# Kernel optimization log

Hardware: AMD Instinct MI355X
Metric: run time of the kernel (lower is better)

## Reference

```python
import jax, jax.numpy as jnp
import numpy as np
from jax import lax

IOU_THRESHOLD = 0.5       # init kwarg
MAX_BOX_PRE_NMS = 1000    # hardcoded in original forward


def _iou_one_vs_all(box, boxes):
    # box: [4] xyxy, boxes: [K,4] xyxy  (torchvision-style IoU, no +1)
    lt = jnp.maximum(box[:2], boxes[:, :2])
    rb = jnp.minimum(box[2:], boxes[:, 2:])
    wh = jnp.clip(rb - lt, 0.0)
    inter = wh[:, 0] * wh[:, 1]
    area1 = (box[2] - box[0]) * (box[3] - box[1])
    area2 = (boxes[:, 2] - boxes[:, 0]) * (boxes[:, 3] - boxes[:, 1])
    return inter / (area1 + area2 - inter)


def _nms_keep(boxes, valid, iou_thr):
    # boxes [K,4] sorted by descending score, valid [K] bool. Greedy NMS:
    # suppress any later box with IoU > iou_thr w.r.t. a kept box.
    K = boxes.shape[0]
    idx = jnp.arange(K)

    def body(i, keep):
        iou = _iou_one_vs_all(boxes[i], boxes)          # [K]
        alive = keep[i] & valid[i]
        suppress = alive & (iou > iou_thr) & (idx > i)
        return keep & ~suppress

    return lax.fori_loop(0, K, body, valid)


def setup_inputs() -> dict:
    key = jax.random.key(0)
    ks = jax.random.split(key, 6)
    B, A, C = 4, 100000, 80
    x = jax.random.normal(ks[0], (B, 3, 64, 64), jnp.float32)
    anchors = jax.random.uniform(ks[1], (1, A, 4), dtype=jnp.float32)
    regression = jax.random.normal(ks[2], (B, A, 4), jnp.float32)
    classification = jax.random.uniform(ks[3], (B, A, C), dtype=jnp.float32)
    # valid xyxy boxes: x2>x1, y2>y1
    xy = jax.random.uniform(ks[4], (B, A, 2), dtype=jnp.float32) * 512.0
    wh = jax.random.uniform(ks[5], (B, A, 2), dtype=jnp.float32) * 64.0 + 1.0
    transformed_anchors = jnp.concatenate([xy, xy + wh], axis=-1)
    return {
        "x": x,
        "anchors": anchors,
        "regression": regression,
        "classification": classification,
        "transformed_anchors": transformed_anchors,
        "threshold": jnp.float32(0.5),
        "max_box": 100,
    }


def reference(x, anchors, regression, classification, transformed_anchors, threshold, max_box):
    # Padded, jit-compatible equivalent of the per-image/per-class loop:
    # rois [B,max_box,4], scores [B,max_box] (0 for padding),
    # class_ids [B,max_box] (-1 for padding).
    B, A, C = classification.shape
    K = MAX_BOX_PRE_NMS
    # threshold gate -> -inf so below-threshold candidates never survive top-k
    scores = jnp.where(classification > threshold, classification, -jnp.inf)  # [B,A,C]
    scores_ct = jnp.swapaxes(scores, 1, 2)                                    # [B,C,A]
    top_s, top_idx = lax.top_k(scores_ct, K)                                  # [B,C,K]
    boxes = jnp.take_along_axis(
        transformed_anchors[:, None], top_idx[..., None], axis=2)             # [B,C,K,4]
    valid = jnp.isfinite(top_s)                                               # [B,C,K]

    keep = jax.vmap(lambda b, v: _nms_keep(b, v, IOU_THRESHOLD))(
        boxes.reshape(B * C, K, 4), valid.reshape(B * C, K)).reshape(B, C, K)

    kept_scores = jnp.where(keep, top_s, -jnp.inf)
    flat_scores = kept_scores.reshape(B, C * K)
    flat_boxes = boxes.reshape(B, C * K, 4)
    class_ids = jnp.broadcast_to(
        jnp.arange(C, dtype=jnp.int32)[:, None], (C, K)).reshape(C * K)

    fin_s, fin_i = lax.top_k(flat_scores, max_box)                            # [B,max_box]
    rois = jnp.take_along_axis(flat_boxes, fin_i[..., None], axis=1)          # [B,max_box,4]
    out_class = class_ids[fin_i]
    out_valid = jnp.isfinite(fin_s)
    rois = jnp.where(out_valid[..., None], rois, 0.0)
    scores_out = jnp.where(out_valid, fin_s, 0.0)
    out_class = jnp.where(out_valid, out_class, -1)
    return rois, scores_out, out_class
```

## Files before the change

### kernel.cpp

```cpp
#include <hip/hip_runtime.h>
#include <hip/hip_bf16.h>

typedef unsigned long long u64;

#define KNMS 1000
#define KP   1024
#define CAP  4096
#define NBIN 8192
#define SLICES 320
#define SCAP 32
#define SLOTS (SLICES*SCAP)
#define CMAX 128
#define FSEL 1024
#define IOU_THR 0.5f

#define NEGINF __uint_as_float(0xFF800000u)


__device__ __forceinline__ void find_cutoff(unsigned int* hist, int nbins,
    unsigned int* csum, int nthreads, int tid, unsigned int rank,
    unsigned int* s_bin, unsigned int* s_gt, unsigned int* s_total, int* s_all) {
  int chunk = nbins / nthreads;
  unsigned int cs = 0;
  int base = tid * chunk;
  for (int q = 0; q < chunk; q++) cs += hist[base + q];
  csum[tid] = cs;
  __syncthreads();
  if (tid == 0) {
    unsigned int total = 0;
    for (int ch = 0; ch < nthreads; ch++) total += csum[ch];
    *s_total = total;
    if (total <= rank) { *s_bin = 0u; *s_gt = 0u; *s_all = 1; }
    else {
      unsigned int acc = 0; int ch = nthreads - 1;
      while (acc + csum[ch] < rank) { acc += csum[ch]; ch--; }
      int bin = ch * chunk + chunk - 1;
      while (acc + hist[bin] < rank) { acc += hist[bin]; bin--; }
      *s_bin = (unsigned)bin; *s_gt = acc; *s_all = 0;
    }
  }
  __syncthreads();
}

template<int N, int NT>
__device__ __forceinline__ void bitonic_desc(u64* a, int tid) {
  for (int k = 2; k <= N; k <<= 1) {
    for (int j = k >> 1; j > 0; j >>= 1) {
      for (int t = tid; t < N; t += NT) {
        int ixj = t ^ j;
        if (ixj > t) {
          u64 x = a[t], y = a[ixj];
          if (((t & k) == 0) ? (x < y) : (x > y)) { a[t] = y; a[ixj] = x; }
        }
      }
      __syncthreads();
    }
  }
}

__device__ __forceinline__ bool iou_gt(float4 bi, float ai, float4 bj, float aj) {
  float ltx = fmaxf(bi.x, bj.x), lty = fmaxf(bi.y, bj.y);
  float rbx = fminf(bi.z, bj.z), rby = fminf(bi.w, bj.w);
  float ww = fmaxf(rbx - ltx, 0.f), hh = fmaxf(rby - lty, 0.f);
  float inter = ww * hh;
  float uni = (ai + aj) - inter;
  float q = (inter + inter) - uni;
  float t = uni * 0x1p-24f;
  return q > t;
}

__global__ __launch_bounds__(1024) void k_sample(const float* __restrict__ cls,
    const float* __restrict__ thr_p, unsigned* __restrict__ gcut,
    float* __restrict__ gatef, unsigned* __restrict__ gflag, int A, int C) {
  int b = blockIdx.x, tid = threadIdx.x;
  __shared__ unsigned hist[CMAX * 64];
  float thr = *thr_p;
  unsigned base_bin = __float_as_uint(thr) >> 18;
  for (int i = tid; i < C * 64; i += 1024) hist[i] = 0u;
  __syncthreads();
  const float* src = cls + (size_t)b * A * C;
  const int NS = 4096;
  if ((C & 3) == 0) {
    int C4 = C >> 2;
    const float4* s4 = (const float4*)src;
    int tot4 = NS * C4;
    for (int idx = tid; idx < tot4; idx += 1024) {
      int s = idx / C4, c4 = idx - s * C4;
      int a = (int)(((long long)s * A) >> 12);
      float4 v = s4[(size_t)a * C4 + c4];
      float vv[4] = {v.x, v.y, v.z, v.w};
#pragma unroll
      for (int q = 0; q < 4; q++) {
        float sv = vv[q];
        if (sv > thr) {
          unsigned rel = (__float_as_uint(sv) >> 18) - base_bin;
          if (rel > 63u) rel = 63u;
          atomicAdd(&hist[(c4 * 4 + q) * 64 + rel], 1u);
        }
      }
    }
  } else {
    int tot = NS * C;
    for (int idx = tid; idx < tot; idx += 1024) {
      int s = idx / C, c = idx - s * C;
      int a = (int)(((long long)s * A) >> 12);
      float sv = src[(size_t)a * C + c];
      if (sv > thr) {
        unsigned rel = (__float_as_uint(sv) >> 18) - base_bin;
        if (rel > 63u) rel = 63u;
        atomicAdd(&hist[c * 64 + rel], 1u);
      }
    }
  }
  __syncthreads();
  if (tid < C) {
    int ns = NS < A ? NS : A;
    long long r = (1500LL * ns) / A; if (r < 1) r = 1;
    unsigned acc = 0; int bin = -1;
    for (int rb = 63; rb >= 0; --rb) {
      acc += hist[tid * 64 + rb];
      if (acc >= (unsigned)r) { bin = rb; break; }
    }
    unsigned cutv = (bin < 0) ? 0u : (base_bin + (unsigned)bin);
    gcut[b * C + tid] = cutv;
    float gate = thr;
    if (cutv != 0u) {
      unsigned cb = cutv << 18;
      if (__uint_as_float(cb) > thr) gate = __uint_as_float(cb - 1u);
    }
    gatef[b * C + tid] = gate;
    gflag[b * C + tid] = 0u;
  }
}

__global__ void k_selA(const float* __restrict__ cls,
    const float* __restrict__ gatef, u64* __restrict__ gcand,
    unsigned* __restrict__ gpc, unsigned* __restrict__ gflag, int A, int C) {
  int slice = blockIdx.x, b = blockIdx.y, tid = threadIdx.x;
  int nt = blockDim.x;
  __shared__ u64 stage[CMAX * SCAP];
  __shared__ unsigned pcnt[CMAX];
  int C4 = C >> 2;
  for (int i = tid; i < C; i += nt) pcnt[i] = 0u;
  __syncthreads();
  int ANC = (A + SLICES - 1) / SLICES;
  int a0 = slice * ANC, a1 = min(A, a0 + ANC);
  int c4 = tid % C4;
  int r0 = tid / C4;
  int R = nt / C4;
  float4 g4 = ((const float4*)(gatef + (size_t)b * C))[c4];
  const float4* p = (const float4*)cls + (size_t)b * A * C4
                    + (size_t)(a0 + r0) * C4 + c4;
  int cb = c4 << 2;
  for (int ar = a0 + r0; ar < a1; ar += R, p += (size_t)R * C4) {
    float4 v = *p;
    bool p0 = v.x > g4.x, p1 = v.y > g4.y, p2 = v.z > g4.z, p3 = v.w > g4.w;
    if (p0 | p1 | p2 | p3) {
      unsigned ia = (unsigned)(~(unsigned)ar);
      if (p0) { unsigned pos = atomicAdd(&pcnt[cb + 0], 1u);
        if (pos < SCAP) stage[(cb + 0) * SCAP + pos] = ((u64)__float_as_uint(v.x) << 32) | ia; }
      if (p1) { unsigned pos = atomicAdd(&pcnt[cb + 1], 1u);
        if (pos < SCAP) stage[(cb + 1) * SCAP + pos] = ((u64)__float_as_uint(v.y) << 32) | ia; }
      if (p2) { unsigned pos = atomicAdd(&pcnt[cb + 2], 1u);
        if (pos < SCAP) stage[(cb + 2) * SCAP + pos] = ((u64)__float_as_uint(v.z) << 32) | ia; }
      if (p3) { unsigned pos = atomicAdd(&pcnt[cb + 3], 1u);
        if (pos < SCAP) stage[(cb + 3) * SCAP + pos] = ((u64)__float_as_uint(v.w) << 32) | ia; }
    }
  }
  __syncthreads();
  for (int idx = tid; idx < C * SCAP; idx += nt) {
    int c = idx >> 5, j = idx & (SCAP - 1);
    unsigned cnt2 = pcnt[c]; if (cnt2 > SCAP) cnt2 = SCAP;
    if ((unsigned)j < cnt2)
      gcand[(size_t)(b * C + c) * SLOTS + slice * SCAP + j] = stage[idx];
  }
  for (int c = tid; c < C; c += nt) {
    unsigned cnt2 = pcnt[c];
    if (cnt2 > SCAP) { atomicOr(&gflag[b * C + c], 1u); cnt2 = SCAP; }
    gpc[(size_t)(b * C + c) * SLICES + slice] = cnt2;
  }
}

__global__ void k_selAs(const float* __restrict__ cls,
    const float* __restrict__ gatef, u64* __restrict__ gcand,
    unsigned* __restrict__ gpc, unsigned* __restrict__ gflag, int A, int C) {
  int slice = blockIdx.x, b = blockIdx.y, tid = threadIdx.x;
  int nt = blockDim.x;
  __shared__ u64 stage[CMAX * SCAP];
  __shared__ unsigned pcnt[CMAX];
  for (int i = tid; i < C; i += nt) pcnt[i] = 0u;
  __syncthreads();
  int ANC = (A + SLICES - 1) / SLICES;
  int a0 = slice * ANC, a1 = min(A, a0 + ANC);
  int c = tid % C;
  int r0 = tid / C;
  int R = nt / C;
  float gate = gatef[(size_t)b * C + c];
  const float* p = cls + (size_t)b * A * C + (size_t)(a0 + r0) * C + c;
  for (int ar = a0 + r0; ar < a1; ar += R, p += (size_t)R * C) {
    float sv = *p;
    if (sv > gate) {
      unsigned pos = atomicAdd(&pcnt[c], 1u);
      if (pos < SCAP)
        stage[c * SCAP + pos] = ((u64)__float_as_uint(sv) << 32) | (unsigned)(~(unsigned)ar);
    }
  }
  __syncthreads();
  for (int idx = tid; idx < C * SCAP; idx += nt) {
    int cc = idx >> 5, j = idx & (SCAP - 1);
    unsigned cnt2 = pcnt[cc]; if (cnt2 > SCAP) cnt2 = SCAP;
    if ((unsigned)j < cnt2)
      gcand[(size_t)(b * C + cc) * SLOTS + slice * SCAP + j] = stage[idx];
  }
  for (int cc = tid; cc < C; cc += nt) {
    unsigned cnt2 = pcnt[cc];
    if (cnt2 > SCAP) { atomicOr(&gflag[b * C + cc], 1u); cnt2 = SCAP; }
    gpc[(size_t)(b * C + cc) * SLICES + slice] = cnt2;
  }
}

__global__ __launch_bounds__(1024) void k_selB(const u64* __restrict__ gcand,
    const unsigned* __restrict__ gpc, const unsigned* __restrict__ gcut,
    const unsigned* __restrict__ gflag, const float* __restrict__ cls,
    const float* __restrict__ thr_p, const float* __restrict__ tanch,
    float* __restrict__ scores_s, float* __restrict__ boxes_s,
    float* __restrict__ area_s, int* __restrict__ cnt_s, int A, int C) {
  int pair = blockIdx.x, tid = threadIdx.x;
  int b = pair / C, c = pair - b * C;
  __shared__ union { unsigned hist[NBIN]; u64 cand[CAP]; } sh;
  __shared__ unsigned cnts[SLICES];
  __shared__ unsigned pre[SLICES];
  __shared__ unsigned csum[1024];
  __shared__ unsigned s_b1, s_gt, s_tot;
  __shared__ int s_all, s_ovf;

  unsigned flag = gflag[pair];
  for (int i = tid; i < SLICES; i += 1024) {
    unsigned v = gpc[(size_t)pair * SLICES + i];
    cnts[i] = v; pre[i] = v;
  }
  __syncthreads();
  for (int d = 1; d < SLICES; d <<= 1) {
    unsigned v = 0;
    if (tid < SLICES && tid >= d) v = pre[tid - d];
    __syncthreads();
    if (tid < SLICES && tid >= d) pre[tid] += v;
    __syncthreads();
  }
  unsigned total = pre[SLICES - 1];
  bool mode_sampled = (gcut[pair] != 0u);
  bool bad = (flag != 0u) || (total > CAP) ||
             (mode_sampled && total < (unsigned)KNMS);
  unsigned n_valid_u;
  if (!bad) {
    for (int t = tid; t < CAP; t += 1024) sh.cand[t] = 0ull;
    __syncthreads();
    const u64* src = gcand + (size_t)pair * SLOTS;
    for (int idx = tid; idx < SLOTS; idx += 1024) {
      int s = idx >> 5, j = idx & (SCAP - 1);
      if ((unsigned)j < cnts[s]) sh.cand[(pre[s] - cnts[s]) + j] = src[idx];
    }
    __syncthreads();
    n_valid_u = total < (unsigned)KNMS ? total : (unsigned)KNMS;
  } else {
    const float* col = cls + (size_t)b * A * C + c;
    float thr = *thr_p;
    for (int i = tid; i < NBIN; i += 1024) sh.hist[i] = 0u;
    __syncthreads();
    for (int a = tid; a < A; a += 1024) {
      float sv = col[(size_t)a * C];
      if (sv > thr) atomicAdd(&sh.hist[__float_as_uint(sv) >> 18], 1u);
    }
    __syncthreads();
    find_cutoff(sh.hist, NBIN, csum, 1024, tid, KNMS, &s_b1, &s_gt, &s_tot, &s_all);
    unsigned b1 = s_all ? 0u : s_b1;
    unsigned tot = s_tot;
    __syncthreads();
    for (int t = tid; t < CAP; t += 1024) sh.cand[t] = 0ull;
    if (tid == 0) s_ovf = 0;
    __syncthreads();
    int lane = tid & 63, wv = tid >> 6;
    u64* seg = sh.cand + wv * 240;
    int nloc = 0;
    u64 lmask = (1ull << lane) - 1ull;
    for (int a = tid; a < A; a += 1024) {
      float sv = col[(size_t)a * C];
      unsigned bits = __float_as_uint(sv);
      bool take = (sv > thr) && ((bits >> 18) >= b1);
      u64 m = __ballot(take);
      if (m) {
        if (take) {
          u64 key = ((u64)bits << 32) | (unsigned)(~(unsigned)a);
          int pos = nloc + (int)__popcll(m & lmask);
          if (pos < 240) seg[pos] = key;
          else { int p2 = atomicAdd(&s_ovf, 1); if (p2 < 256) sh.cand[16 * 240 + p2] = key; }
        }
        nloc += (int)__popcll(m);
      }
    }
    __syncthreads();
    n_valid_u = tot < (unsigned)KNMS ? tot : (unsigned)KNMS;
  }

  bitonic_desc<CAP, 1024>(sh.cand, tid);

  int n_valid = (int)n_valid_u;
  for (int k = tid; k < KNMS; k += 1024) {
    u64 key = sh.cand[k];
    float sc; float4 bx; float ar;
    if (k < n_valid && key != 0ull) {
      sc = __uint_as_float((unsigned)(key >> 32));
      unsigned a = ~(unsigned)key;
      bx = ((const float4*)tanch)[(size_t)b * A + a];
      ar = (bx.z - bx.x) * (bx.w - bx.y);
    } else {
      sc = NEGINF; bx = make_float4(0.f, 0.f, 0.f, 0.f); ar = 0.f;
    }
    scores_s[(size_t)pair * KP + k] = sc;
    ((float4*)boxes_s)[(size_t)pair * KP + k] = bx;
    area_s[(size_t)pair * KP + k] = ar;
  }
  if (tid == 0) cnt_s[pair] = n_valid;
}

__global__ __launch_bounds__(256) void k_iou(const float* __restrict__ boxes_s,
    const int* __restrict__ cnt_s, u64* __restrict__ mat) {
  int pair = blockIdx.x, g = blockIdx.y;
  int Ac = g, Bc = 15 - g;
  int cnt = cnt_s[pair];
  __shared__ float4 sbox[KNMS];
  __shared__ u64 rowm[2][KP];
  for (int i = threadIdx.x; i < KNMS; i += 256)
    sbox[i] = ((const float4*)boxes_s)[(size_t)pair * KP + i];
  {
    u64* rz = &rowm[0][0];
    for (int i = threadIdx.x; i < 2 * KP; i += 256) rz[i] = 0ull;
  }
  __syncthreads();
  int lane = threadIdx.x & 63;
  int wv = __builtin_amdgcn_readfirstlane(threadIdx.x >> 6);
  float4 z4 = make_float4(0.f, 0.f, 0.f, 0.f);
  float4 biA = sbox[Ac * 64 + lane];
  int ib = Bc * 64 + lane;
  float4 biB = (ib < KNMS) ? sbox[ib] : z4;
  float aiA = (biA.z - biA.x) * (biA.w - biA.y);
  float aiB = (biB.z - biB.x) * (biB.w - biB.y);
  int lim = cnt;
  int e1 = Ac * 64 + 64; if (e1 > lim) e1 = lim;
  for (int j = Ac * 64 + 1 + wv; j < e1; j += 4) {
    float4 bj = sbox[j];
    float aj = (bj.z - bj.x) * (bj.w - bj.y);
    u64 mk = (1ull << (j - Ac * 64)) - 1ull;
    u64 w0 = __ballot(iou_gt(biA, aiA, bj, aj)) & mk;
    if (lane == 0) rowm[0][j] = w0;
  }
  int s2e = Bc * 64 + 1; if (s2e > lim) s2e = lim;
  for (int j = Ac * 64 + 64 + (wv << 1); j < s2e; j += 8) {
    float4 bj0 = sbox[j];
    bool h2 = (j + 1 < s2e);
    float4 bj1 = h2 ? sbox[j + 1] : z4;
    float aj0 = (bj0.z - bj0.x) * (bj0.w - bj0.y);
    float aj1 = (bj1.z - bj1.x) * (bj1.w - bj1.y);
    u64 w00 = __ballot(iou_gt(biA, aiA, bj0, aj0));
    u64 w01 = __ballot(iou_gt(biA, aiA, bj1, aj1));
    if (lane == 0) { rowm[0][j] = w00; if (h2) rowm[0][j + 1] = w01; }
  }
  int e3 = Bc * 64 + 64; if (e3 > lim) e3 = lim;
  for (int j = Bc * 64 + 1 + wv; j < e3; j += 4) {
    float4 bj = sbox[j];
    float aj = (bj.z - bj.x) * (bj.w - bj.y);
    u64 w0 = __ballot(iou_gt(biA, aiA, bj, aj));
    u64 mk = (1ull << (j - Bc * 64)) - 1ull;
    u64 w1 = __ballot(iou_gt(biB, aiB, bj, aj)) & mk;
    if (lane == 0) { rowm[0][j] = w0; rowm[1][j] = w1; }
  }
  for (int j = Bc * 64 + 64 + (wv << 1); j < lim; j += 8) {
    float4 bj0 = sbox[j];
    bool h2 = (j + 1 < lim);
    float4 bj1 = h2 ? sbox[j + 1] : z4;
    float aj0 = (bj0.z - bj0.x) * (bj0.w - bj0.y);
    float aj1 = (bj1.z - bj1.x) * (bj1.w - bj1.y);
    u64 w00 = __ballot(iou_gt(biA, aiA, bj0, aj0));
    u64 w10 = __ballot(iou_gt(biB, aiB, bj0, aj0));
    u64 w01 = __ballot(iou_gt(biA, aiA, bj1, aj1));
    u64 w11 = __ballot(iou_gt(biB, aiB, bj1, aj1));
    if (lane == 0) {
      rowm[0][j] = w00; rowm[1][j] = w10;
      if (h2) { rowm[0][j + 1] = w01; rowm[1][j + 1] = w11; }
    }
  }
  __syncthreads();
  {
    u64* dstA = mat + ((size_t)pair * 16 + Ac) * KP;
    for (int t = Ac * 64 + threadIdx.x; t < cnt; t += 256) dstA[t] = rowm[0][t];
    u64* dstB = mat + ((size_t)pair * 16 + Bc) * KP;
    for (int t = Bc * 64 + threadIdx.x; t < cnt; t += 256) dstB[t] = rowm[1][t];
  }
}

__global__ __launch_bounds__(64) void k_scanfa(const u64* __restrict__ mat,
    const int* __restrict__ cnt_s, const float* __restrict__ scores_s,
    u64* __restrict__ fa, int C, int mb) {
  int pair = blockIdx.x;
  int l = threadIdx.x;
  int cnt = cnt_s[pair];
  const u64* cm = mat + (size_t)pair * KP * 16;
  u64 supw = 0ull;
  u64 kfin = 0ull;
  for (int t = 0; t < 16; t++) {
    int base = t * 64;
    if (base >= cnt) break;
    int nb = cnt - base; if (nb > 64) nb = 64;
    u64 validt = (nb >= 64) ? ~0ull : ((1ull << nb) - 1ull);
    const u64* cmt = cm + (size_t)t * KP;
    u64 dg = cmt[base + l];
    u64 v[15];
#pragma unroll
    for (int q = 0; q < 15; q++) {
      int jw = t + 1 + q;
      v[q] = (jw < 16 && jw * 64 < cnt) ? cmt[jw * 64 + l] : 0ull;
    }
    u64 supt = __shfl(supw, t);
    u64 rem = validt & ~supt;
    u64 nz = __ballot(dg != 0ull) & rem;
    u64 keep = rem & ~nz;
    while (nz) {
      int i = __ffsll((long long)nz) - 1;
      nz &= nz - 1;
      u64 di = __shfl(dg, i);
      if ((di & keep) == 0ull) keep |= 1ull << i;
    }
    if (l == t) kfin = keep;
#pragma unroll
    for (int q = 0; q < 15; q++) {
      int jw = t + 1 + q;
      if (jw < 16) {
        u64 bal = __ballot((v[q] & keep) != 0ull);
        if (l == jw) supw |= bal;
      }
    }
  }
  int c = pair % C;
  int pc = __popcll(kfin);
  int scan = pc;
  for (int d = 1; d < 16; d <<= 1) {
    int o = __shfl_up(scan, d);
    if (l >= d) scan += o;
  }
  int basep = scan - pc;
  int total = __shfl(scan, 15);
  if (l < 16) {
    u64 mm = kfin; int r = basep;
    while (mm && r < mb) {
      int bit = __ffsll((long long)mm) - 1; mm &= mm - 1;
      int k = l * 64 + bit;
      float s = scores_s[(size_t)pair * KP + k];
      fa[(size_t)pair * mb + r] =
          ((u64)__float_as_uint(s) << 32) | (unsigned)(~(unsigned)(c * KNMS + k));
      r++;
    }
  }
  int start = total < mb ? total : mb;
  for (int r = start + l; r < mb; r += 64) fa[(size_t)pair * mb + r] = 0ull;
}

__global__ __launch_bounds__(1024) void k_fb(const u64* __restrict__ fa,
    const float* __restrict__ boxes_s, float* __restrict__ out,
    int B, int C, int mb) {
  int b = blockIdx.x, tid = threadIdx.x;
  __shared__ union { unsigned int hist[NBIN]; u64 cand[FSEL]; } sh;
  __shared__ unsigned int csum[1024];
  __shared__ unsigned int s_b1, s_gt, s_tot, s_b2, s_gt2, s_tot2;
  __shared__ int s_all, s_all2, s_n, s_lvl2;
  int nk = C * mb;
  const u64* src = fa + (size_t)b * nk;

  for (int i = tid; i < NBIN; i += 1024) sh.hist[i] = 0u;
  __syncthreads();
  for (int i = tid; i < nk; i += 1024) {
    u64 key = src[i];
    if (key) atomicAdd(&sh.hist[(unsigned)(key >> 32) >> 18], 1u);
  }
  __syncthreads();
  find_cutoff(sh.hist, NBIN, csum, 1024, tid, (unsigned)mb, &s_b1, &s_gt, &s_tot, &s_all);
  unsigned b1 = s_all ? 0u : s_b1;
  unsigned gt1 = s_gt, tot = s_tot;
  int all1 = s_all;
  unsigned m1 = sh.hist[b1];
  if (tid == 0) s_lvl2 = (!all1 && gt1 + m1 > FSEL) ? 1 : 0;
  __syncthreads();
  int lvl2 = s_lvl2;
  unsigned b2 = 0; int all2 = 1;
  if (lvl2) {
    for (int i = tid; i < 2048; i += 1024) sh.hist[i] = 0u;
    __syncthreads();
    for (int i = tid; i < nk; i += 1024) {
      u64 key = src[i];
      if (key) {
        unsigned bits = (unsigned)(key >> 32);
        if ((bits >> 18) == b1) atomicAdd(&sh.hist[(bits >> 7) & 2047u], 1u);
      }
    }
    __syncthreads();
    find_cutoff(sh.hist, 2048, csum, 1024, tid, (unsigned)mb - gt1,
                &s_b2, &s_gt2, &s_tot2, &s_all2);
    all2 = s_all2;
    b2 = all2 ? 0u : s_b2;
  }
  for (int t = tid; t < FSEL; t += 1024) sh.cand[t] = 0ull;
  if (tid == 0) s_n = 0;
  __syncthreads();
  for (int i = tid; i < nk; i += 1024) {
    u64 key = src[i];
    if (!key) continue;
    unsigned bits = (unsigned)(key >> 32);
    unsigned bin = bits >> 18;
    bool take = all1 || bin > b1 ||
                (bin == b1 && (!lvl2 || all2 || ((bits >> 7) & 2047u) >= b2));
    if (take) {
      int pos = atomicAdd(&s_n, 1);
      if (pos < FSEL) sh.cand[pos] = key;
    }
  }
  __syncthreads();
  bitonic_desc<FSEL, 1024>(sh.cand, tid);

  int n_out = (int)tot < mb ? (int)tot : mb;
  for (int k = tid; k < mb; k += 1024) {
    u64 key = sh.cand[k];
    float4 bx = make_float4(0.f, 0.f, 0.f, 0.f);
    float sc = 0.f, cf = -1.f;
    if (k < n_out && key != 0ull) {
      sc = __uint_as_float((unsigned)(key >> 32));
      unsigned flat = ~(unsigned)key;
      int c = flat / KNMS;
      int kk = flat - c * KNMS;
      bx = ((const float4*)boxes_s)[(size_t)(b * C + c) * KP + kk];
      cf = (float)c;
    }
    size_t ro = (size_t)(b * mb + k) * 4;
    out[ro + 0] = bx.x; out[ro + 1] = bx.y; out[ro + 2] = bx.z; out[ro + 3] = bx.w;
    out[(size_t)B * mb * 4 + b * mb + k] = sc;
    out[(size_t)B * mb * 5 + b * mb + k] = cf;
  }
}

extern "C" void kernel_launch(void* const* d_in, const int* in_sizes, int n_in,
                              void* d_out, int out_size, void* d_ws, size_t ws_size,
                              hipStream_t stream) {
  const float* classification = (const float*)d_in[3];
  const float* tanch = (const float*)d_in[4];
  const float* thr_p = (const float*)d_in[5];

  int B = in_sizes[0] / (3 * 64 * 64);
  if (B <= 0) B = 4;
  long long BA = (long long)in_sizes[4] / 4;
  int A = (int)(BA / B);
  int C = (int)((long long)in_sizes[3] / BA);
  int NP = B * C;
  int mb = out_size / (B * 6);

  auto rsz = [](size_t x) { return (x + 255) & ~(size_t)255; };
  size_t off = 0;
  auto take = [&](size_t bytes) {
    void* p = (char*)d_ws + off;
    off += rsz(bytes);
    return p;
  };
  float* scores_s = (float*)take((size_t)NP * KP * 4);
  float* boxes_s  = (float*)take((size_t)NP * KP * 16);
  float* area_s   = (float*)take((size_t)NP * KP * 4);
  int*   cnt_s    = (int*)take((size_t)NP * 4);
  u64*   mat      = (u64*)take((size_t)NP * KP * 16 * 8);

  char* matc = (char*)mat;
  size_t ao = 0;
  u64* gcand      = (u64*)(matc + ao);      ao += rsz((size_t)NP * SLOTS * 8);
  unsigned* gpc   = (unsigned*)(matc + ao); ao += rsz((size_t)NP * SLICES * 4);
  unsigned* gcut  = (unsigned*)(matc + ao); ao += rsz((size_t)NP * 4);
  unsigned* gflag = (unsigned*)(matc + ao); ao += rsz((size_t)NP * 4);
  float* gatef    = (float*)(matc + ao);    ao += rsz((size_t)NP * 4);
  u64* fa = (u64*)area_s;

  int fastsel = (C <= CMAX) ? 1 : 0;

  if (fastsel) {
    k_sample<<<B, 1024, 0, stream>>>(classification, thr_p, gcut, gatef, gflag, A, C);
    if ((C & 3) == 0) {
      int C4 = C >> 2;
      int R = 512 / C4; if (R < 1) R = 1;
      k_selA<<<dim3(SLICES, B), C4 * R, 0, stream>>>(classification, gatef,
                                                     gcand, gpc, gflag, A, C);
    } else {
      int R = 512 / C; if (R < 1) R = 1;
      k_selAs<<<dim3(SLICES, B), C * R, 0, stream>>>(classification, gatef,
                                                     gcand, gpc, gflag, A, C);
    }
  } else {
    hipMemsetAsync(gflag, 1, (size_t)NP * 4, stream);
    hipMemsetAsync(gcut, 0, (size_t)NP * 4, stream);
  }
  k_selB<<<NP, 1024, 0, stream>>>(gcand, gpc, gcut, gflag, classification, thr_p,
                                  tanch, scores_s, boxes_s, area_s, cnt_s, A, C);
  k_iou<<<dim3(NP, 8), 256, 0, stream>>>(boxes_s, cnt_s, mat);
  k_scanfa<<<NP, 64, 0, stream>>>(mat, cnt_s, scores_s, fa, C, mb);
  k_fb<<<B, 1024, 0, stream>>>(fa, boxes_s, (float*)d_out, B, C, mb);
}
```

Measured before the change: 366.0 us.

## Prefilter candidates via radix histogram before bitonic sort in selection kernel

In the fast path of the per-(image,class) selection kernel, candidates are binned into a 64-bin histogram relative to the sampled gate value, with an optional second-level 2048-bin histogram. This locates the cutoff for the top 1000, and only keys at or above it are compacted into a 1024-entry buffer, so the bitonic sort runs on 1024 elements instead of 4096. It falls back to the full sort when the key range is wide or the cutoff bin would overflow. It also drops the unused area output write. The trade is extra shared memory and more histogram passes and barriers, which may lower occupancy.

```diff
diff --git a/kernel.cpp b/kernel.cpp
--- a/kernel.cpp
+++ b/kernel.cpp
@@ -221,18 +221,23 @@
 
 __global__ __launch_bounds__(1024) void k_selB(const u64* __restrict__ gcand,
     const unsigned* __restrict__ gpc, const unsigned* __restrict__ gcut,
-    const unsigned* __restrict__ gflag, const float* __restrict__ cls,
-    const float* __restrict__ thr_p, const float* __restrict__ tanch,
+    const unsigned* __restrict__ gflag, const float* __restrict__ gatef,
+    const float* __restrict__ cls, const float* __restrict__ thr_p,
+    const float* __restrict__ tanch,
     float* __restrict__ scores_s, float* __restrict__ boxes_s,
-    float* __restrict__ area_s, int* __restrict__ cnt_s, int A, int C) {
+    int* __restrict__ cnt_s, int A, int C) {
   int pair = blockIdx.x, tid = threadIdx.x;
   int b = pair / C, c = pair - b * C;
   __shared__ union { unsigned hist[NBIN]; u64 cand[CAP]; } sh;
+  __shared__ u64 cand2[1024];
+  __shared__ unsigned h2[2048];
+  __shared__ unsigned hw[16][64];
+  __shared__ unsigned hist64[64];
   __shared__ unsigned cnts[SLICES];
   __shared__ unsigned pre[SLICES];
   __shared__ unsigned csum[1024];
-  __shared__ unsigned s_b1, s_gt, s_tot;
-  __shared__ int s_all, s_ovf;
+  __shared__ unsigned s_b1, s_gt, s_tot, s_b2, s_gt2, s_tot2;
+  __shared__ int s_all, s_all2, s_ovf, s_mode, s_lvl2, s_wide, s_ntake;
 
   unsigned flag = gflag[pair];
   for (int i = tid; i < SLICES; i += 1024) {
@@ -252,6 +257,7 @@
   bool bad = (flag != 0u) || (total > CAP) ||
              (mode_sampled && total < (unsigned)KNMS);
   unsigned n_valid_u;
+  bool fullsort;
   if (!bad) {
     for (int t = tid; t < CAP; t += 1024) sh.cand[t] = 0ull;
     __syncthreads();
@@ -260,9 +266,85 @@
       int s = idx >> 5, j = idx & (SCAP - 1);
       if ((unsigned)j < cnts[s]) sh.cand[(pre[s] - cnts[s]) + j] = src[idx];
     }
-    __syncthreads();
     n_valid_u = total < (unsigned)KNMS ? total : (unsigned)KNMS;
+    unsigned base = __float_as_uint(gatef[pair]) >> 18;
+    for (int i = tid; i < 16 * 64; i += 1024) (&hw[0][0])[i] = 0u;
+    if (tid == 0) { s_wide = 0; s_ntake = 0; }
+    __syncthreads();
+    int wv = tid >> 6;
+    for (int t = tid; t < CAP; t += 1024) {
+      u64 key = sh.cand[t];
+      if (!key) continue;
+      unsigned rel = ((unsigned)(key >> 32) >> 18) - base;
+      if (rel > 63u) s_wide = 1;
+      else atomicAdd(&hw[wv][rel], 1u);
+    }
+    __syncthreads();
+    if (tid < 64) {
+      unsigned s = 0;
+#pragma unroll
+      for (int w = 0; w < 16; w++) s += hw[w][tid];
+      hist64[tid] = s;
+    }
+    __syncthreads();
+    if (tid == 0) {
+      int mode = 0; unsigned b1 = 0, gt = 0; int lvl2 = 0;
+      if (s_wide) mode = 2;
+      else if (total > (unsigned)KNMS) {
+        unsigned acc = 0; int bin = 63;
+        for (; bin > 0; --bin) {
+          unsigned h = hist64[bin];
+          if (acc + h >= (unsigned)KNMS) break;
+          acc += h;
+        }
+        b1 = (unsigned)bin; gt = acc;
+        if (gt + hist64[b1] > 1024u) lvl2 = 1;
+      }
+      s_b1 = b1; s_gt = gt; s_mode = mode; s_lvl2 = lvl2;
+    }
+    __syncthreads();
+    unsigned b1v = s_b1, gtv = s_gt;
+    int lvl2 = s_lvl2;
+    unsigned b2v = 0;
+    if (s_mode == 0 && lvl2) {
+      for (int i = tid; i < 2048; i += 1024) h2[i] = 0u;
+      __syncthreads();
+      for (int t = tid; t < CAP; t += 1024) {
+        u64 key = sh.cand[t];
+        if (!key) continue;
+        unsigned bits = (unsigned)(key >> 32);
+        if (((bits >> 18) - base) == b1v)
+          atomicAdd(&h2[(bits >> 7) & 2047u], 1u);
+      }
+      __syncthreads();
+      find_cutoff(h2, 2048, csum, 1024, tid, (unsigned)KNMS - gtv,
+                  &s_b2, &s_gt2, &s_tot2, &s_all2);
+      if (tid == 0) {
+        if (s_all2 || gtv + s_gt2 + h2[s_b2] > 1024u) s_mode = 2;
+      }
+      __syncthreads();
+      b2v = s_all2 ? 0u : s_b2;
+    }
+    fullsort = (s_mode == 2);
+    if (!fullsort) {
+      if (tid < 1024) cand2[tid] = 0ull;
+      __syncthreads();
+      for (int t = tid; t < CAP; t += 1024) {
+        u64 key = sh.cand[t];
+        if (!key) continue;
+        unsigned bits = (unsigned)(key >> 32);
+        unsigned rel = (bits >> 18) - base;
+        bool take = rel > b1v ||
+                    (rel == b1v && (!lvl2 || ((bits >> 7) & 2047u) >= b2v));
+        if (take) {
+          int pos = atomicAdd(&s_ntake, 1);
+          if (pos < 1024) cand2[pos] = key;
+        }
+      }
+      __syncthreads();
+    }
   } else {
+    fullsort = true;
     const float* col = cls + (size_t)b * A * C + c;
     float thr = *thr_p;
     for (int i = tid; i < NBIN; i += 1024) sh.hist[i] = 0u;
@@ -302,23 +384,23 @@
     n_valid_u = tot < (unsigned)KNMS ? tot : (unsigned)KNMS;
   }
 
-  bitonic_desc<CAP, 1024>(sh.cand, tid);
+  if (fullsort) bitonic_desc<CAP, 1024>(sh.cand, tid);
+  else          bitonic_desc<1024, 1024>(cand2, tid);
+  const u64* osrc = fullsort ? (const u64*)sh.cand : (const u64*)cand2;
 
   int n_valid = (int)n_valid_u;
   for (int k = tid; k < KNMS; k += 1024) {
-    u64 key = sh.cand[k];
-    float sc; float4 bx; float ar;
+    u64 key = osrc[k];
+    float sc; float4 bx;
     if (k < n_valid && key != 0ull) {
       sc = __uint_as_float((unsigned)(key >> 32));
       unsigned a = ~(unsigned)key;
       bx = ((const float4*)tanch)[(size_t)b * A + a];
-      ar = (bx.z - bx.x) * (bx.w - bx.y);
     } else {
-      sc = NEGINF; bx = make_float4(0.f, 0.f, 0.f, 0.f); ar = 0.f;
+      sc = NEGINF; bx = make_float4(0.f, 0.f, 0.f, 0.f);
     }
     scores_s[(size_t)pair * KP + k] = sc;
     ((float4*)boxes_s)[(size_t)pair * KP + k] = bx;
-    area_s[(size_t)pair * KP + k] = ar;
   }
   if (tid == 0) cnt_s[pair] = n_valid;
 }
@@ -357,13 +439,13 @@
   int s2e = Bc * 64 + 1; if (s2e > lim) s2e = lim;
   for (int j = Ac * 64 + 64 + (wv << 1); j < s2e; j += 8) {
     float4 bj0 = sbox[j];
-    bool h2 = (j + 1 < s2e);
-    float4 bj1 = h2 ? sbox[j + 1] : z4;
+    bool h2b = (j + 1 < s2e);
+    float4 bj1 = h2b ? sbox[j + 1] : z4;
     float aj0 = (bj0.z - bj0.x) * (bj0.w - bj0.y);
     float aj1 = (bj1.z - bj1.x) * (bj1.w - bj1.y);
     u64 w00 = __ballot(iou_gt(biA, aiA, bj0, aj0));
     u64 w01 = __ballot(iou_gt(biA, aiA, bj1, aj1));
-    if (lane == 0) { rowm[0][j] = w00; if (h2) rowm[0][j + 1] = w01; }
+    if (lane == 0) { rowm[0][j] = w00; if (h2b) rowm[0][j + 1] = w01; }
   }
   int e3 = Bc * 64 + 64; if (e3 > lim) e3 = lim;
   for (int j = Bc * 64 + 1 + wv; j < e3; j += 4) {
@@ -376,8 +458,8 @@
   }
   for (int j = Bc * 64 + 64 + (wv << 1); j < lim; j += 8) {
     float4 bj0 = sbox[j];
-    bool h2 = (j + 1 < lim);
-    float4 bj1 = h2 ? sbox[j + 1] : z4;
+    bool h2b = (j + 1 < lim);
+    float4 bj1 = h2b ? sbox[j + 1] : z4;
     float aj0 = (bj0.z - bj0.x) * (bj0.w - bj0.y);
     float aj1 = (bj1.z - bj1.x) * (bj1.w - bj1.y);
     u64 w00 = __ballot(iou_gt(biA, aiA, bj0, aj0));
@@ -386,7 +468,7 @@
     u64 w11 = __ballot(iou_gt(biB, aiB, bj1, aj1));
     if (lane == 0) {
       rowm[0][j] = w00; rowm[1][j] = w10;
-      if (h2) { rowm[0][j + 1] = w01; rowm[1][j + 1] = w11; }
+      if (h2b) { rowm[0][j + 1] = w01; rowm[1][j + 1] = w11; }
     }
   }
   __syncthreads();
@@ -599,9 +681,10 @@
   } else {
     hipMemsetAsync(gflag, 1, (size_t)NP * 4, stream);
     hipMemsetAsync(gcut, 0, (size_t)NP * 4, stream);
-  }
-  k_selB<<<NP, 1024, 0, stream>>>(gcand, gpc, gcut, gflag, classification, thr_p,
-                                  tanch, scores_s, boxes_s, area_s, cnt_s, A, C);
+    hipMemsetAsync(gatef, 0, (size_t)NP * 4, stream);
+  }
+  k_selB<<<NP, 1024, 0, stream>>>(gcand, gpc, gcut, gflag, gatef, classification,
+                                  thr_p, tanch, scores_s, boxes_s, cnt_s, A, C);
   k_iou<<<dim3(NP, 8), 256, 0, stream>>>(boxes_s, cnt_s, mat);
   k_scanfa<<<NP, 64, 0, stream>>>(mat, cnt_s, scores_s, fa, C, mb);
   k_fb<<<B, 1024, 0, stream>>>(fa, boxes_s, (float*)d_out, B, C, mb);
```

Measured after the change: 351.4 us. -4.0%, faster.
